# Kernel tuning notes

Hardware: AMD Instinct MI355X
Metric: run time of the kernel (lower is better)

The kernel has to match this reference:

```python
import jax, jax.numpy as jnp
import numpy as np

B, T, C = 4, 2048, 1024
H = 16
HD = C // H  # head_dim = 64


def setup_inputs() -> dict:
    key = jax.random.key(0)
    k1, k2, k3 = jax.random.split(key, 3)
    x = jax.random.normal(k1, (B, T, C), dtype=jnp.float32)
    # nn.Linear weights stored as (out_features, in_features); y = x @ W.T
    w_qkv = jax.random.normal(k2, (3 * C, C), dtype=jnp.float32) * (1.0 / np.sqrt(C))
    w_out = jax.random.normal(k3, (C, C), dtype=jnp.float32) * (1.0 / np.sqrt(C))
    return {"x": x, "w_qkv": w_qkv, "w_out": w_out}


def reference(x, w_qkv, w_out):
    Bb, Tt, Cc = x.shape
    qkv = jnp.einsum('btc,oc->bto', x, w_qkv)  # (B,T,3C)
    q, k, v = jnp.split(qkv, 3, axis=2)
    # (B,T,H,HD) -> (B,H,T,HD)
    q = q.reshape(Bb, Tt, H, HD).transpose(0, 2, 1, 3)
    k = k.reshape(Bb, Tt, H, HD).transpose(0, 2, 1, 3)
    v = v.reshape(Bb, Tt, H, HD).transpose(0, 2, 1, 3)
    scores = jnp.einsum('bhqd,bhkd->bhqk', q, k) / jnp.sqrt(jnp.float32(HD))
    causal = jnp.tril(jnp.ones((Tt, Tt), dtype=bool))  # True = keep
    scores = jnp.where(causal[None, None], scores, jnp.float32(-jnp.inf))
    weights = jax.nn.softmax(scores, axis=-1)
    att = jnp.einsum('bhqk,bhkd->bhqd', weights, v)  # (B,H,T,HD)
    att = att.transpose(0, 2, 1, 3).reshape(Bb, Tt, Cc)
    return jnp.einsum('btc,oc->bto', att, w_out)
```

## Files before the change

### kernel.cpp

```cpp
#include <hip/hip_runtime.h>
#include <hip/hip_bf16.h>

#define B_   4
#define T_   2048
#define C_   1024
#define H_   16
#define HD_  64
#define M_   8192
#define N1_  3072
#define N2_  1024

typedef __attribute__((ext_vector_type(8))) short bf16x8;
typedef __attribute__((ext_vector_type(4))) float f32x4;

static __device__ __forceinline__ unsigned short f2bf(float f) {
  union { float f; unsigned u; } cv; cv.f = f;
  unsigned u = cv.u;
  return (unsigned short)((u + 0x7FFFu + ((u >> 16) & 1u)) >> 16);
}

static __device__ __forceinline__ float exp2_fast(float x) {
  float r;
  asm("v_exp_f32 %0, %1" : "=v"(r) : "v"(x));
  return r;
}

static __device__ __forceinline__ unsigned cvt_pk_bf16(float lo, float hi) {
  unsigned r;
  asm("v_cvt_pk_bf16_f32 %0, %1, %2" : "=v"(r) : "v"(lo), "v"(hi));
  return r;
}

#define AS1 __attribute__((address_space(1)))
#define AS3 __attribute__((address_space(3)))
static __device__ __forceinline__ void gload_lds16(const void* g, void* l) {
  __builtin_amdgcn_global_load_lds((const AS1 void*)g, (AS3 void*)l, 16, 0, 0);
}

#define N4_X  (M_ * C_ / 4)
#define N4_WQ (N1_ * C_ / 4)
#define N4_WO (N2_ * C_ / 4)
__global__ void cast_all_kernel(const float* __restrict__ x, const float* __restrict__ wq,
                                const float* __restrict__ wo,
                                unsigned short* __restrict__ xb, unsigned short* __restrict__ wqb,
                                unsigned short* __restrict__ wob) {
  int stride = gridDim.x * blockDim.x;
  for (int i = blockIdx.x * blockDim.x + threadIdx.x; i < N4_X + N4_WQ + N4_WO; i += stride) {
    const float* src; unsigned short* dst; int j;
    if (i < N4_X)            { src = x;  dst = xb;  j = i; }
    else if (i < N4_X + N4_WQ) { src = wq; dst = wqb; j = i - N4_X; }
    else                     { src = wo; dst = wob; j = i - N4_X - N4_WQ; }
    f32x4 v = ((const f32x4*)src)[j];
    ushort4 o;
    o.x = f2bf(v[0]); o.y = f2bf(v[1]); o.z = f2bf(v[2]); o.w = f2bf(v[3]);
    ((ushort4*)dst)[j] = o;
  }
}

__global__ __launch_bounds__(512, 2) void gemm_qkv(
    const unsigned short* __restrict__ Xb,
    const unsigned short* __restrict__ Wb,
    unsigned short* __restrict__ Qb,
    unsigned short* __restrict__ Kb,
    unsigned short* __restrict__ Vtb)
{
  __shared__ __align__(16) unsigned short As[2][256 * 64];
  __shared__ __align__(16) unsigned short Bs[2][256 * 64];
  const int tid  = threadIdx.x;
  const int lane = tid & 63;
  const int wave = tid >> 6;
  const int rowgrp = wave >> 1;
  const int colgrp = wave & 1;
  const int g = lane >> 4, q4 = lane & 15;
  const int row0 = blockIdx.x * 256;
  const int col0 = blockIdx.y * 256;
  const int NT = C_ / 64;

  const int cb0 = wave * 128;
  const int cb1 = wave * 128 + 64;
  const int c0 = cb0 + lane, c1 = cb1 + lane;
  const int r0s = c0 >> 3, j0 = (c0 & 7) ^ (r0s & 7);
  const int r1s = c1 >> 3, j1 = (c1 & 7) ^ (r1s & 7);
  const unsigned short* xs0 = Xb + (size_t)(row0 + r0s) * C_ + j0 * 8;
  const unsigned short* xs1 = Xb + (size_t)(row0 + r1s) * C_ + j1 * 8;
  const unsigned short* ws0 = Wb + (size_t)(col0 + r0s) * C_ + j0 * 8;
  const unsigned short* ws1 = Wb + (size_t)(col0 + r1s) * C_ + j1 * 8;

  auto stage = [&](int t, int h, int isB) {
    const int buf = t & 1;
    const size_t hoff = (size_t)h * 128 * C_;
    const int k0 = t * 64;
    const unsigned short* s0 = (isB ? ws0 : xs0) + hoff + k0;
    const unsigned short* s1 = (isB ? ws1 : xs1) + hoff + k0;
    char* dbase = (char*)(isB ? Bs[buf] : As[buf]) + h * 1024 * 16;
    gload_lds16(s0, dbase + cb0 * 16);
    gload_lds16(s1, dbase + cb1 * 16);
  };

  bf16x8 aA[2][2], aB[2][2], bb[4][2];
  auto readA = [&](bf16x8 (&a)[2][2], int buf, int h) {
    #pragma unroll
    for (int mt = 0; mt < 2; ++mt) {
      int row = h * 128 + rowgrp * 32 + mt * 16 + q4;
      #pragma unroll
      for (int ks = 0; ks < 2; ++ks) {
        int byte = (row * 128 + (ks * 32 + g * 8) * 2) ^ ((row & 7) << 4);
        a[mt][ks] = *(const bf16x8*)((const char*)As[buf] + byte);
      }
    }
  };
  auto readB = [&](int buf, int h) {
    #pragma unroll
    for (int nt = 0; nt < 4; ++nt) {
      int row = h * 128 + colgrp * 64 + nt * 16 + q4;
      #pragma unroll
      for (int ks = 0; ks < 2; ++ks) {
        int byte = (row * 128 + (ks * 32 + g * 8) * 2) ^ ((row & 7) << 4);
        bb[nt][ks] = *(const bf16x8*)((const char*)Bs[buf] + byte);
      }
    }
  };

  f32x4 zero = {0.f, 0.f, 0.f, 0.f};
  f32x4 acc00[2][4], acc10[2][4], acc11[2][4], acc01[2][4];
  #pragma unroll
  for (int m = 0; m < 2; ++m)
    #pragma unroll
    for (int n = 0; n < 4; ++n) { acc00[m][n] = zero; acc10[m][n] = zero; acc11[m][n] = zero; acc01[m][n] = zero; }

  auto mfma16 = [&](f32x4 (&ac)[2][4], bf16x8 (&a)[2][2]) {
    __builtin_amdgcn_s_setprio(1);
    #pragma unroll
    for (int mt = 0; mt < 2; ++mt)
      #pragma unroll
      for (int nt = 0; nt < 4; ++nt)
        #pragma unroll
        for (int ks = 0; ks < 2; ++ks)
          ac[mt][nt] = __builtin_amdgcn_mfma_f32_16x16x32_bf16(a[mt][ks], bb[nt][ks], ac[mt][nt], 0, 0, 0);
    __builtin_amdgcn_s_setprio(0);
  };

  stage(0, 0, 0); stage(0, 0, 1); stage(0, 1, 0); stage(0, 1, 1);
  asm volatile("s_waitcnt vmcnt(0)" ::: "memory");
  __builtin_amdgcn_s_barrier();
  __builtin_amdgcn_sched_barrier(0);

  for (int t = 0; t < NT - 1; ++t) {
    const int buf = t & 1;
    readA(aA, buf, 0);
    readB(buf, 0);
    stage(t + 1, 0, 0);
    asm volatile("s_waitcnt lgkmcnt(0)" ::: "memory");
    __builtin_amdgcn_sched_barrier(0);
    mfma16(acc00, aA);
    asm volatile("s_waitcnt vmcnt(4)" ::: "memory");
    __builtin_amdgcn_s_barrier();
    __builtin_amdgcn_sched_barrier(0);
    readA(aB, buf, 1);
    stage(t + 1, 0, 1);
    asm volatile("s_waitcnt lgkmcnt(0)" ::: "memory");
    __builtin_amdgcn_sched_barrier(0);
    mfma16(acc10, aB);
    asm volatile("s_waitcnt vmcnt(4)" ::: "memory");
    __builtin_amdgcn_s_barrier();
    __builtin_amdgcn_sched_barrier(0);
    readB(buf, 1);
    stage(t + 1, 1, 0);
    asm volatile("s_waitcnt lgkmcnt(0)" ::: "memory");
    __builtin_amdgcn_sched_barrier(0);
    mfma16(acc11, aB);
    asm volatile("s_waitcnt vmcnt(4)" ::: "memory");
    __builtin_amdgcn_s_barrier();
    __builtin_amdgcn_sched_barrier(0);
    stage(t + 1, 1, 1);
    mfma16(acc01, aA);
    asm volatile("s_waitcnt vmcnt(4)" ::: "memory");
    __builtin_amdgcn_s_barrier();
    __builtin_amdgcn_sched_barrier(0);
  }
  {
    const int buf = (NT - 1) & 1;
    readA(aA, buf, 0);
    readB(buf, 0);
    asm volatile("s_waitcnt lgkmcnt(0)" ::: "memory");
    __builtin_amdgcn_sched_barrier(0);
    mfma16(acc00, aA);
    asm volatile("s_waitcnt vmcnt(2)" ::: "memory");
    __builtin_amdgcn_s_barrier();
    __builtin_amdgcn_sched_barrier(0);
    readA(aB, buf, 1);
    asm volatile("s_waitcnt lgkmcnt(0)" ::: "memory");
    __builtin_amdgcn_sched_barrier(0);
    mfma16(acc10, aB);
    asm volatile("s_waitcnt vmcnt(0)" ::: "memory");
    __builtin_amdgcn_s_barrier();
    __builtin_amdgcn_sched_barrier(0);
    readB(buf, 1);
    asm volatile("s_waitcnt lgkmcnt(0)" ::: "memory");
    __builtin_amdgcn_sched_barrier(0);
    mfma16(acc11, aB);
    mfma16(acc01, aA);
  }

  const float SC = 0.125f * 1.44269504f;
  #pragma unroll
  for (int qr = 0; qr < 2; ++qr) {
    #pragma unroll
    for (int qc = 0; qc < 2; ++qc) {
      #pragma unroll
      for (int mt = 0; mt < 2; ++mt) {
        #pragma unroll
        for (int nt = 0; nt < 4; ++nt) {
          f32x4 v = (qr == 0) ? ((qc == 0) ? acc00[mt][nt] : acc01[mt][nt])
                              : ((qc == 0) ? acc10[mt][nt] : acc11[mt][nt]);
          int col = col0 + qc * 128 + colgrp * 64 + nt * 16 + q4;
          int which = col >> 10;
          int cc = col & 1023;
          int h = cc >> 6, d = cc & 63;
          int r0 = row0 + qr * 128 + rowgrp * 32 + mt * 16 + g * 4;
          int bb_ = r0 >> 11, t0 = r0 & 2047;
          if (which == 2) {
            uint2 pk;
            pk.x = cvt_pk_bf16(v[0], v[1]);
            pk.y = cvt_pk_bf16(v[2], v[3]);
            *(uint2*)(Vtb + (((size_t)(bb_ * 16 + h)) * 64 + d) * T_ + t0) = pk;
          } else {
            unsigned short* dst = (which == 0) ? Qb : Kb;
            float sc = (which == 0) ? SC : 1.f;
            #pragma unroll
            for (int rg = 0; rg < 4; ++rg)
              dst[(((size_t)(bb_ * 16 + h)) * T_ + t0 + rg) * 64 + d] = f2bf(v[rg] * sc);
          }
        }
      }
    }
  }
}

__global__ __launch_bounds__(256, 3) void attn_kernel(
    const unsigned short* __restrict__ Qb,
    const unsigned short* __restrict__ Kb,
    const unsigned short* __restrict__ Vtb,
    unsigned short* __restrict__ Ob)
{
  __shared__ __align__(16) unsigned short Ks[2][64 * 64];
  __shared__ __align__(16) unsigned short Vs[2][64 * 64];
  __shared__ __align__(16) unsigned short Ps[4][32 * 64];
  const int tid  = threadIdx.x;
  const int lane = tid & 63;
  const int wave = tid >> 6;
  const int g = lane >> 4, q4 = lane & 15;
  const int bh = blockIdx.x;
  const int qt = 15 - blockIdx.y;
  const unsigned short* Qp = Qb  + (size_t)bh * T_ * 64;
  const unsigned short* Kp = Kb  + (size_t)bh * T_ * 64;
  const unsigned short* Vp = Vtb + (size_t)bh * 64 * T_;
  const int qb = qt * 128 + wave * 32;
  const int nT = 2 * qt + 2;
  const int nKeys = qb + 31;

  bf16x8 qf[2][2];
  #pragma unroll
  for (int qtl = 0; qtl < 2; ++qtl)
    #pragma unroll
    for (int ks = 0; ks < 2; ++ks)
      qf[qtl][ks] = *(const bf16x8*)(Qp + (size_t)(qb + qtl * 16 + q4) * 64 + ks * 32 + g * 8);

  bf16x8 ones;
  #pragma unroll
  for (int i = 0; i < 8; ++i) ones[i] = (short)0x3F80;

  f32x4 zero = {0.f, 0.f, 0.f, 0.f};
  f32x4 oacc[2][4], lacc[2];
  #pragma unroll
  for (int i = 0; i < 2; ++i) {
    lacc[i] = zero;
    #pragma unroll
    for (int jj = 0; jj < 4; ++jj) oacc[i][jj] = zero;
  }
  float m_run[2] = {-1e30f, -1e30f};
  const float THR = 10.0f;

  auto stage = [&](int t, int buf) {
    const int kv0 = t * 64;
    #pragma unroll
    for (int i = 0; i < 2; ++i) {
      int cb = wave * 128 + i * 64;
      int c  = cb + lane;
      int r  = c >> 3;
      int jx = (c & 7) ^ (r & 7);
      gload_lds16(Kp + (size_t)(kv0 + r) * 64 + jx * 8, (char*)Ks[buf] + cb * 16);
      gload_lds16(Vp + (size_t)r * T_ + kv0 + jx * 8,   (char*)Vs[buf] + cb * 16);
    }
  };

  stage(0, 0);
  for (int t = 0; t < nT; ++t) {
    asm volatile("s_waitcnt vmcnt(0)" ::: "memory");
    __builtin_amdgcn_s_barrier();
    __builtin_amdgcn_sched_barrier(0);
    if (t + 1 < nT) stage(t + 1, (t + 1) & 1);
    const int cur = t & 1;
    const int kv0 = t * 64;
    if (kv0 > nKeys) continue;

    f32x4 s[4][2];
    #pragma unroll
    for (int mt = 0; mt < 4; ++mt)
      #pragma unroll
      for (int qtl = 0; qtl < 2; ++qtl) s[mt][qtl] = zero;
    #pragma unroll
    for (int ks = 0; ks < 2; ++ks) {
      bf16x8 kf[4];
      #pragma unroll
      for (int mt = 0; mt < 4; ++mt) {
        int row = mt * 16 + q4;
        int byte = (row * 128 + (ks * 32 + g * 8) * 2) ^ ((row & 7) << 4);
        kf[mt] = *(const bf16x8*)((const char*)Ks[cur] + byte);
      }
      __builtin_amdgcn_s_setprio(1);
      #pragma unroll
      for (int mt = 0; mt < 4; ++mt)
        #pragma unroll
        for (int qtl = 0; qtl < 2; ++qtl)
          s[mt][qtl] = __builtin_amdgcn_mfma_f32_16x16x32_bf16(kf[mt], qf[qtl][ks], s[mt][qtl], 0, 0, 0);
      __builtin_amdgcn_s_setprio(0);
    }

    const bool needMask = (kv0 + 63 > qb);
    if (needMask) {
      #pragma unroll
      for (int mt = 0; mt < 4; ++mt)
        #pragma unroll
        for (int qtl = 0; qtl < 2; ++qtl)
          #pragma unroll
          for (int rg = 0; rg < 4; ++rg) {
            int key = kv0 + mt * 16 + g * 4 + rg;
            int qrow = qb + qtl * 16 + q4;
            s[mt][qtl][rg] = (key <= qrow) ? s[mt][qtl][rg] : -1e30f;
          }
    }
    float tmax[2];
    #pragma unroll
    for (int qtl = 0; qtl < 2; ++qtl) {
      float mm[4];
      #pragma unroll
      for (int mt = 0; mt < 4; ++mt)
        mm[mt] = fmaxf(fmaxf(s[mt][qtl][0], s[mt][qtl][1]),
                       fmaxf(s[mt][qtl][2], s[mt][qtl][3]));
      float tm = fmaxf(fmaxf(mm[0], mm[1]), fmaxf(mm[2], mm[3]));
      tm = fmaxf(tm, __shfl_xor(tm, 16, 64));
      tm = fmaxf(tm, __shfl_xor(tm, 32, 64));
      tmax[qtl] = tm;
    }
    if (!__all((tmax[0] <= m_run[0] + THR) & (tmax[1] <= m_run[1] + THR))) {
      #pragma unroll
      for (int qtl = 0; qtl < 2; ++qtl) {
        float mnew = fmaxf(m_run[qtl], tmax[qtl]);
        float alpha = exp2_fast(m_run[qtl] - mnew);
        m_run[qtl] = mnew;
        float al[4];
        #pragma unroll
        for (int rg = 0; rg < 4; ++rg) al[rg] = __shfl(alpha, g * 4 + rg, 64);
        #pragma unroll
        for (int dt = 0; dt < 4; ++dt)
          #pragma unroll
          for (int rg = 0; rg < 4; ++rg) oacc[qtl][dt][rg] *= al[rg];
        #pragma unroll
        for (int rg = 0; rg < 4; ++rg) lacc[qtl][rg] *= al[rg];
      }
    }
    #pragma unroll
    for (int qtl = 0; qtl < 2; ++qtl)
      #pragma unroll
      for (int mt = 0; mt < 4; ++mt) {
        float p0 = exp2_fast(s[mt][qtl][0] - m_run[qtl]);
        float p1 = exp2_fast(s[mt][qtl][1] - m_run[qtl]);
        float p2 = exp2_fast(s[mt][qtl][2] - m_run[qtl]);
        float p3 = exp2_fast(s[mt][qtl][3] - m_run[qtl]);
        uint2 pk;
        pk.x = cvt_pk_bf16(p0, p1);
        pk.y = cvt_pk_bf16(p2, p3);
        int row = qtl * 16 + q4;
        int byte = (row * 128 + (mt * 16 + g * 4) * 2) ^ ((row & 7) << 4);
        *(uint2*)((char*)Ps[wave] + byte) = pk;
      }
    #pragma unroll
    for (int ks = 0; ks < 2; ++ks) {
      bf16x8 pf[2], vf[4];
      #pragma unroll
      for (int qtl = 0; qtl < 2; ++qtl) {
        int row = qtl * 16 + q4;
        int byte = (row * 128 + (ks * 32 + g * 8) * 2) ^ ((row & 7) << 4);
        pf[qtl] = *(const bf16x8*)((const char*)Ps[wave] + byte);
      }
      #pragma unroll
      for (int dt = 0; dt < 4; ++dt) {
        int row = dt * 16 + q4;
        int byte = (row * 128 + (ks * 32 + g * 8) * 2) ^ ((row & 7) << 4);
        vf[dt] = *(const bf16x8*)((const char*)Vs[cur] + byte);
      }
      __builtin_amdgcn_s_setprio(1);
      #pragma unroll
      for (int qtl = 0; qtl < 2; ++qtl) {
        #pragma unroll
        for (int dt = 0; dt < 4; ++dt)
          oacc[qtl][dt] = __builtin_amdgcn_mfma_f32_16x16x32_bf16(pf[qtl], vf[dt], oacc[qtl][dt], 0, 0, 0);
        lacc[qtl] = __builtin_amdgcn_mfma_f32_16x16x32_bf16(pf[qtl], ones, lacc[qtl], 0, 0, 0);
      }
      __builtin_amdgcn_s_setprio(0);
    }
  }

  #pragma unroll
  for (int qtl = 0; qtl < 2; ++qtl) {
    #pragma unroll
    for (int dt = 0; dt < 4; ++dt) {
      #pragma unroll
      for (int rg = 0; rg < 4; ++rg) {
        int tq = qb + qtl * 16 + g * 4 + rg;
        int d = dt * 16 + q4;
        Ob[((size_t)bh * T_ + tq) * 64 + d] = f2bf(oacc[qtl][dt][rg] / lacc[qtl][rg]);
      }
    }
  }
}

__global__ __launch_bounds__(256, 3) void gemm_out(
    const unsigned short* __restrict__ Ob,
    const unsigned short* __restrict__ Wo,
    float* __restrict__ Out)
{
  __shared__ __align__(16) unsigned short As[3][128 * 32];
  __shared__ __align__(16) unsigned short Bs[3][128 * 32];
  const int tid  = threadIdx.x;
  const int lane = tid & 63;
  const int wave = tid >> 6;
  const int wr = wave >> 1, wc = wave & 1;
  const int g = lane >> 4, q4 = lane & 15;
  const int row0 = blockIdx.x * 128;
  const int col0 = blockIdx.y * 128;
  const int NT = C_ / 32;

  auto stage = [&](int kt) {
    const int buf = kt % 3;
    const int k0 = kt * 32;
    #pragma unroll
    for (int i = 0; i < 2; ++i) {
      int cb = wave * 128 + i * 64;
      int c  = cb + lane;
      int r  = c >> 2;
      int j  = (c & 3) ^ ((r >> 1) & 3);
      int rr = row0 + r;
      int cc = k0 + j * 8;
      const unsigned short* srcA =
          Ob + (((size_t)((rr >> 11) * 16 + (cc >> 6))) * T_ + (rr & 2047)) * 64 + (cc & 63);
      gload_lds16(srcA, (char*)As[buf] + cb * 16);
      gload_lds16(Wo + (size_t)(col0 + r) * C_ + cc, (char*)Bs[buf] + cb * 16);
    }
  };

  f32x4 zero = {0.f, 0.f, 0.f, 0.f};
  f32x4 acc[4][4];
  for (int i = 0; i < 4; ++i) for (int j = 0; j < 4; ++j) acc[i][j] = zero;

  auto ktile = [&](int buf) {
    bf16x8 a[4], b[4];
    #pragma unroll
    for (int im = 0; im < 4; ++im) {
      int row = wr * 64 + im * 16 + q4;
      a[im] = *(const bf16x8*)((const char*)As[buf] + row * 64 + ((g ^ ((row >> 1) & 3)) * 16));
    }
    #pragma unroll
    for (int in_ = 0; in_ < 4; ++in_) {
      int row = wc * 64 + in_ * 16 + q4;
      b[in_] = *(const bf16x8*)((const char*)Bs[buf] + row * 64 + ((g ^ ((row >> 1) & 3)) * 16));
    }
    __builtin_amdgcn_s_setprio(1);
    #pragma unroll
    for (int im = 0; im < 4; ++im)
      #pragma unroll
      for (int in_ = 0; in_ < 4; ++in_)
        acc[im][in_] = __builtin_amdgcn_mfma_f32_16x16x32_bf16(a[im], b[in_], acc[im][in_], 0, 0, 0);
    __builtin_amdgcn_s_setprio(0);
  };

  stage(0); stage(1);
  for (int kt = 0; kt < NT - 1; ++kt) {
    asm volatile("s_waitcnt vmcnt(4)" ::: "memory");
    __builtin_amdgcn_s_barrier();
    __builtin_amdgcn_sched_barrier(0);
    if (kt + 2 < NT) stage(kt + 2);
    ktile(kt % 3);
  }
  asm volatile("s_waitcnt vmcnt(0)" ::: "memory");
  __builtin_amdgcn_s_barrier();
  __builtin_amdgcn_sched_barrier(0);
  ktile((NT - 1) % 3);

  #pragma unroll
  for (int im = 0; im < 4; ++im)
    #pragma unroll
    for (int in_ = 0; in_ < 4; ++in_) {
      int col = col0 + wc * 64 + in_ * 16 + q4;
      #pragma unroll
      for (int rg = 0; rg < 4; ++rg) {
        int r = row0 + wr * 64 + im * 16 + g * 4 + rg;
        Out[(size_t)r * C_ + col] = acc[im][in_][rg];
      }
    }
}

extern "C" void kernel_launch(void* const* d_in, const int* in_sizes, int n_in,
                              void* d_out, int out_size, void* d_ws, size_t ws_size,
                              hipStream_t stream) {
  const float* x     = (const float*)d_in[0];
  const float* w_qkv = (const float*)d_in[1];
  const float* w_out = (const float*)d_in[2];
  float* out = (float*)d_out;
  char* ws = (char*)d_ws;
  unsigned short* xb  = (unsigned short*)(ws);
  unsigned short* wqb = (unsigned short*)(ws + 16777216);
  unsigned short* wob = (unsigned short*)(ws + 16777216 + 6291456);
  unsigned short* Qb  = (unsigned short*)(ws + 25165824);
  unsigned short* Kb  = (unsigned short*)(ws + 25165824 + 16777216);
  unsigned short* Vtb = (unsigned short*)(ws + 25165824 + 2 * 16777216);
  unsigned short* Ob  = (unsigned short*)(ws + 25165824 + 3 * 16777216);

  cast_all_kernel<<<2048, 256, 0, stream>>>(x, w_qkv, w_out, xb, wqb, wob);
  gemm_qkv<<<dim3(M_ / 256, N1_ / 256), 512, 0, stream>>>(xb, wqb, Qb, Kb, Vtb);
  attn_kernel<<<dim3(B_ * H_, 16), 256, 0, stream>>>(Qb, Kb, Vtb, Ob);
  gemm_out<<<dim3(M_ / 128, N2_ / 128), 256, 0, stream>>>(Ob, wob, out);
}
```

Measured before the change: 168.6 us.

## Split LDS reads by k-step and swizzle QKV GEMM block order

Measured after the change: 180.5 us. 1.07x slower.

```diff
diff --git a/kernel.cpp b/kernel.cpp
--- a/kernel.cpp
+++ b/kernel.cpp
@@ -72,8 +72,10 @@
   const int rowgrp = wave >> 1;
   const int colgrp = wave & 1;
   const int g = lane >> 4, q4 = lane & 15;
-  const int row0 = blockIdx.x * 256;
-  const int col0 = blockIdx.y * 256;
+  const int lin = blockIdx.y * 32 + blockIdx.x;
+  const int swz = (lin & 7) * 48 + (lin >> 3);
+  const int row0 = (swz & 31) * 256;
+  const int col0 = (swz >> 5) * 256;
   const int NT = C_ / 64;
 
   const int cb0 = wave * 128;
@@ -98,26 +100,20 @@
   };
 
   bf16x8 aA[2][2], aB[2][2], bb[4][2];
-  auto readA = [&](bf16x8 (&a)[2][2], int buf, int h) {
+  auto readAks = [&](bf16x8 (&a)[2][2], int buf, int h, int ks) {
     #pragma unroll
     for (int mt = 0; mt < 2; ++mt) {
       int row = h * 128 + rowgrp * 32 + mt * 16 + q4;
-      #pragma unroll
-      for (int ks = 0; ks < 2; ++ks) {
-        int byte = (row * 128 + (ks * 32 + g * 8) * 2) ^ ((row & 7) << 4);
-        a[mt][ks] = *(const bf16x8*)((const char*)As[buf] + byte);
-      }
-    }
-  };
-  auto readB = [&](int buf, int h) {
+      int byte = (row * 128 + (ks * 32 + g * 8) * 2) ^ ((row & 7) << 4);
+      a[mt][ks] = *(const bf16x8*)((const char*)As[buf] + byte);
+    }
+  };
+  auto readBks = [&](int buf, int h, int ks) {
     #pragma unroll
     for (int nt = 0; nt < 4; ++nt) {
       int row = h * 128 + colgrp * 64 + nt * 16 + q4;
-      #pragma unroll
-      for (int ks = 0; ks < 2; ++ks) {
-        int byte = (row * 128 + (ks * 32 + g * 8) * 2) ^ ((row & 7) << 4);
-        bb[nt][ks] = *(const bf16x8*)((const char*)Bs[buf] + byte);
-      }
+      int byte = (row * 128 + (ks * 32 + g * 8) * 2) ^ ((row & 7) << 4);
+      bb[nt][ks] = *(const bf16x8*)((const char*)Bs[buf] + byte);
     }
   };
 
@@ -128,79 +124,108 @@
     #pragma unroll
     for (int n = 0; n < 4; ++n) { acc00[m][n] = zero; acc10[m][n] = zero; acc11[m][n] = zero; acc01[m][n] = zero; }
 
-  auto mfma16 = [&](f32x4 (&ac)[2][4], bf16x8 (&a)[2][2]) {
+  auto mfma8 = [&](f32x4 (&ac)[2][4], bf16x8 (&a)[2][2], int ks) {
     __builtin_amdgcn_s_setprio(1);
     #pragma unroll
     for (int mt = 0; mt < 2; ++mt)
       #pragma unroll
       for (int nt = 0; nt < 4; ++nt)
-        #pragma unroll
-        for (int ks = 0; ks < 2; ++ks)
-          ac[mt][nt] = __builtin_amdgcn_mfma_f32_16x16x32_bf16(a[mt][ks], bb[nt][ks], ac[mt][nt], 0, 0, 0);
+        ac[mt][nt] = __builtin_amdgcn_mfma_f32_16x16x32_bf16(a[mt][ks], bb[nt][ks], ac[mt][nt], 0, 0, 0);
     __builtin_amdgcn_s_setprio(0);
   };
 
+  #define SB0() __builtin_amdgcn_sched_barrier(0)
+  #define LGKM(n) asm volatile("s_waitcnt lgkmcnt(" #n ")" ::: "memory")
+  #define VMC(n)  asm volatile("s_waitcnt vmcnt(" #n ")" ::: "memory")
+
   stage(0, 0, 0); stage(0, 0, 1); stage(0, 1, 0); stage(0, 1, 1);
-  asm volatile("s_waitcnt vmcnt(0)" ::: "memory");
+  VMC(0);
   __builtin_amdgcn_s_barrier();
-  __builtin_amdgcn_sched_barrier(0);
+  SB0();
 
   for (int t = 0; t < NT - 1; ++t) {
     const int buf = t & 1;
-    readA(aA, buf, 0);
-    readB(buf, 0);
     stage(t + 1, 0, 0);
-    asm volatile("s_waitcnt lgkmcnt(0)" ::: "memory");
-    __builtin_amdgcn_sched_barrier(0);
-    mfma16(acc00, aA);
-    asm volatile("s_waitcnt vmcnt(4)" ::: "memory");
-    __builtin_amdgcn_s_barrier();
-    __builtin_amdgcn_sched_barrier(0);
-    readA(aB, buf, 1);
+    readAks(aA, buf, 0, 0); readBks(buf, 0, 0);
+    SB0();
+    readAks(aA, buf, 0, 1); readBks(buf, 0, 1);
+    SB0();
+    LGKM(6); SB0();
+    mfma8(acc00, aA, 0);
+    LGKM(0); SB0();
+    mfma8(acc00, aA, 1);
+    VMC(4);
+    __builtin_amdgcn_s_barrier();
+    SB0();
     stage(t + 1, 0, 1);
-    asm volatile("s_waitcnt lgkmcnt(0)" ::: "memory");
-    __builtin_amdgcn_sched_barrier(0);
-    mfma16(acc10, aB);
-    asm volatile("s_waitcnt vmcnt(4)" ::: "memory");
-    __builtin_amdgcn_s_barrier();
-    __builtin_amdgcn_sched_barrier(0);
-    readB(buf, 1);
+    readAks(aB, buf, 1, 0);
+    SB0();
+    readAks(aB, buf, 1, 1);
+    SB0();
+    LGKM(2); SB0();
+    mfma8(acc10, aB, 0);
+    LGKM(0); SB0();
+    mfma8(acc10, aB, 1);
+    VMC(4);
+    __builtin_amdgcn_s_barrier();
+    SB0();
     stage(t + 1, 1, 0);
-    asm volatile("s_waitcnt lgkmcnt(0)" ::: "memory");
-    __builtin_amdgcn_sched_barrier(0);
-    mfma16(acc11, aB);
-    asm volatile("s_waitcnt vmcnt(4)" ::: "memory");
-    __builtin_amdgcn_s_barrier();
-    __builtin_amdgcn_sched_barrier(0);
+    readBks(buf, 1, 0);
+    SB0();
+    readBks(buf, 1, 1);
+    SB0();
+    LGKM(4); SB0();
+    mfma8(acc11, aB, 0);
+    LGKM(0); SB0();
+    mfma8(acc11, aB, 1);
+    VMC(4);
+    __builtin_amdgcn_s_barrier();
+    SB0();
     stage(t + 1, 1, 1);
-    mfma16(acc01, aA);
-    asm volatile("s_waitcnt vmcnt(4)" ::: "memory");
-    __builtin_amdgcn_s_barrier();
-    __builtin_amdgcn_sched_barrier(0);
+    mfma8(acc01, aA, 0);
+    mfma8(acc01, aA, 1);
+    VMC(4);
+    __builtin_amdgcn_s_barrier();
+    SB0();
   }
   {
     const int buf = (NT - 1) & 1;
-    readA(aA, buf, 0);
-    readB(buf, 0);
-    asm volatile("s_waitcnt lgkmcnt(0)" ::: "memory");
-    __builtin_amdgcn_sched_barrier(0);
-    mfma16(acc00, aA);
-    asm volatile("s_waitcnt vmcnt(2)" ::: "memory");
-    __builtin_amdgcn_s_barrier();
-    __builtin_amdgcn_sched_barrier(0);
-    readA(aB, buf, 1);
-    asm volatile("s_waitcnt lgkmcnt(0)" ::: "memory");
-    __builtin_amdgcn_sched_barrier(0);
-    mfma16(acc10, aB);
-    asm volatile("s_waitcnt vmcnt(0)" ::: "memory");
-    __builtin_amdgcn_s_barrier();
-    __builtin_amdgcn_sched_barrier(0);
-    readB(buf, 1);
-    asm volatile("s_waitcnt lgkmcnt(0)" ::: "memory");
-    __builtin_amdgcn_sched_barrier(0);
-    mfma16(acc11, aB);
-    mfma16(acc01, aA);
-  }
+    readAks(aA, buf, 0, 0); readBks(buf, 0, 0);
+    SB0();
+    readAks(aA, buf, 0, 1); readBks(buf, 0, 1);
+    SB0();
+    LGKM(6); SB0();
+    mfma8(acc00, aA, 0);
+    LGKM(0); SB0();
+    mfma8(acc00, aA, 1);
+    VMC(2);
+    __builtin_amdgcn_s_barrier();
+    SB0();
+    readAks(aB, buf, 1, 0);
+    SB0();
+    readAks(aB, buf, 1, 1);
+    SB0();
+    LGKM(2); SB0();
+    mfma8(acc10, aB, 0);
+    LGKM(0); SB0();
+    mfma8(acc10, aB, 1);
+    VMC(0);
+    __builtin_amdgcn_s_barrier();
+    SB0();
+    readBks(buf, 1, 0);
+    SB0();
+    readBks(buf, 1, 1);
+    SB0();
+    LGKM(4); SB0();
+    mfma8(acc11, aB, 0);
+    LGKM(0); SB0();
+    mfma8(acc11, aB, 1);
+    mfma8(acc01, aA, 0);
+    mfma8(acc01, aA, 1);
+  }
+  #undef SB0
+  #undef LGKM
+  #undef VMC
 
   const float SC = 0.125f * 1.44269504f;
   #pragma unroll
```
